# Kernel tuning notes

Hardware: AMD Instinct MI355X
Metric: run time of the kernel (lower is better)

The kernel has to match this reference:

```python
import jax, jax.numpy as jnp
import numpy as np

I, H, M, C, LOC, K = 512, 256, 80, 1024, 32, 31
C2 = C // 2
B, S, T = 32, 256, 800


def setup_inputs() -> dict:
    key = jax.random.key(0)
    ks = jax.random.split(key, 20)
    sc = 0.02
    return {
        "encodings": jax.random.normal(ks[0], (B, S, I), jnp.float32),
        "queries": jax.random.normal(ks[1], (B, T, H), jnp.float32),
        "outputs": jax.random.normal(ks[2], (B, T, M), jnp.float32),
        "mask": jnp.ones((B, S), jnp.float32),
        # GRUCell (PyTorch layout: gates ordered r, z, n)
        "w_ih": jax.random.normal(ks[3], (3 * C, I + H), jnp.float32) * sc,
        "w_hh": jax.random.normal(ks[4], (3 * C, C), jnp.float32) * sc,
        "b_ih": jax.random.normal(ks[5], (3 * C,), jnp.float32) * sc,
        "b_hh": jax.random.normal(ks[6], (3 * C,), jnp.float32) * sc,
        "w_q": jax.random.normal(ks[7], (C2, C), jnp.float32) * sc,        # proj_query
        "w_loc1": jax.random.normal(ks[8], (LOC, 1, K), jnp.float32) * sc, # Conv1d(1, loc, K)
        "w_loc2": jax.random.normal(ks[9], (C2, LOC), jnp.float32) * sc,   # Conv1d(loc, C2, 1)
        "w_k": jax.random.normal(ks[10], (C2, I), jnp.float32) * sc,       # proj_key
        "b_k": jax.random.normal(ks[11], (C2,), jnp.float32) * sc,
        "w_agg": jax.random.normal(ks[12], (C2,), jnp.float32) * sc,       # Conv1d(C2, 1, 1)
        "w_t1": jax.random.normal(ks[13], (C, I + C + M), jnp.float32) * sc,
        "b_t1": jax.random.normal(ks[14], (C,), jnp.float32) * sc,
        "w_t2": jax.random.normal(ks[15], (C,), jnp.float32) * sc,
    }


def _conv1d(x, w, pad):
    # x: [B, Cin, S], w: [Cout, Cin, K]
    return jax.lax.conv_general_dilated(
        x, w, window_strides=(1,), padding=[(pad, pad)],
        dimension_numbers=("NCH", "OIH", "NCH"))


def _aligner(encodings, queries, outputs, maskb,
             w_ih, w_hh, b_ih, b_hh, w_q, w_loc1, w_loc2, w_k, b_k,
             w_agg, w_t1, b_t1, w_t2):
    bsize, seqlen, _ = encodings.shape
    # key projection: [B, S, C2]
    key = encodings @ w_k.T + b_k
    h0 = jnp.zeros((bsize, C), encodings.dtype)
    align0 = jnp.full((bsize, seqlen), 1.0 / seqlen, encodings.dtype)
    alpha0 = jnp.zeros((bsize, seqlen), encodings.dtype).at[:, 0].set(1.0)
    trans0 = jnp.full((bsize, 1), 0.5, encodings.dtype)

    def step(carry, xt):
        h, align, trans, alpha = carry
        query, frame = xt  # [B,H], [B,M]
        prev = jnp.einsum("bsi,bs->bi", encodings, alpha)
        x = jnp.concatenate([query, prev], axis=-1)  # [B, H+I]
        gx = x @ w_ih.T + b_ih
        gh = h @ w_hh.T + b_hh
        xr, xz, xn = jnp.split(gx, 3, axis=-1)
        hr, hz, hn = jnp.split(gh, 3, axis=-1)
        r = jax.nn.sigmoid(xr + hr)
        z = jax.nn.sigmoid(xz + hz)
        n = jnp.tanh(xn + r * hn)
        h_new = (1.0 - z) * n + z * h  # GRUCell update
        # location features: [B,1,S] -> [B,LOC,S] -> [B,C2,S]
        loc = _conv1d(align[:, None, :], w_loc1, K // 2)
        loc = jnp.einsum("cl,bls->bcs", w_loc2, loc)
        score = loc + (h_new @ w_q.T)[..., None] + key.swapaxes(1, 2)  # [B,C2,S]
        energy = jnp.einsum("c,bcs->bs", w_agg, jnp.tanh(score))
        energy = jnp.where(maskb, -jnp.inf, energy)
        align_new = jax.nn.softmax(energy, axis=-1)
        shifted = jnp.pad(alpha, ((0, 0), (1, 0)))[:, :-1]  # F.pad(alpha, [1,-1])
        alpha_new = ((1.0 - trans) * alpha + trans * shifted + 1e-7) * align_new
        alpha_new = alpha_new / alpha_new.sum(axis=-1, keepdims=True)
        attend = jnp.einsum("bsi,bs->bi", encodings, alpha_new)
        t_in = jnp.concatenate([attend, frame, h_new], axis=-1)
        t = jax.nn.sigmoid(jnp.tanh(t_in @ w_t1.T + b_t1) @ w_t2[:, None])  # [B,1]
        return (h_new, align_new, t, alpha_new), alpha_new

    xs = (queries.swapaxes(0, 1), outputs.swapaxes(0, 1))
    _, alphas = jax.lax.scan(step, (h0, align0, trans0, alpha0), xs)
    return alphas.swapaxes(0, 1)  # [B, T, S]


def reference(encodings, queries, outputs, mask,
              w_ih, w_hh, b_ih, b_hh, w_q, w_loc1, w_loc2, w_k, b_k,
              w_agg, w_t1, b_t1, w_t2):
    maskb = ~(mask.astype(bool))
    return _aligner(encodings, queries, outputs, maskb,
                    w_ih, w_hh, b_ih, b_hh, w_q, w_loc1, w_loc2, w_k, b_k,
                    w_agg, w_t1, b_t1, w_t2)
```

## Files before the change

kernel.cpp:

```cpp
#include <hip/hip_runtime.h>
#include <cstdint>
#include <cstddef>


namespace cfg {
constexpr int NB = 32, NS = 256, NI = 512, NHq = 256, NM = 80;
constexpr int NC = 1024, NC2 = 512, NT = 800;
constexpr int NBLK = 256, NTHR = 512;

constexpr size_t OFF_KEYT  = 0;
constexpr size_t OFF_WKT   = OFF_KEYT + (size_t)NB * NS * NC2;
constexpr size_t OFF_PU    = OFF_WKT + (size_t)NI * NC2;
constexpr size_t OFF_H     = OFF_PU + (size_t)2 * NB * NI;
constexpr size_t OFF_H16   = OFF_H + (size_t)2 * NC * NB;
constexpr size_t OFF_E     = OFF_H16 + (size_t)NB * NC;
constexpr size_t OFF_W     = OFF_E + (size_t)2 * NB * NS;
constexpr size_t OFF_SE    = OFF_W + (size_t)2 * NB * NS;
constexpr size_t OFF_SW    = OFF_SE + 64;
constexpr size_t OFF_TPART = OFF_SW + 64;
constexpr size_t OFF_TRED  = OFF_TPART + (size_t)NBLK * NB;
constexpr size_t OFF_QBUF  = OFF_TRED + 32;
constexpr size_t OFF_BAR   = OFF_QBUF + (size_t)NB * NC2;
constexpr size_t OFF_Q16   = OFF_BAR + 4608;
constexpr size_t OFF_F16   = OFF_Q16 + (size_t)NT * NB * NHq / 2;
constexpr size_t OFF_WQ16  = OFF_F16 + (size_t)NT * NB * 128 / 2;
constexpr size_t WS_FLOATS = OFF_WQ16 + (size_t)NC2 * NC / 2;
}
using namespace cfg;

typedef __attribute__((ext_vector_type(8))) short short8;
typedef __attribute__((ext_vector_type(4))) float f32x4;

#define MF(a, b, c) __builtin_amdgcn_mfma_f32_16x16x32_bf16((a), (b), (c), 0, 0, 0)
#define LDSC(d, p) asm volatile("global_load_dwordx4 %0, %1, off sc0 sc1" : "=v"(d) : "v"(p))

__device__ __forceinline__ float ld_cg(const float* p) {
  return __hip_atomic_load(p, __ATOMIC_RELAXED, __HIP_MEMORY_SCOPE_AGENT);
}
__device__ __forceinline__ void st_cg(float* p, float v) {
  __hip_atomic_store(p, v, __ATOMIC_RELAXED, __HIP_MEMORY_SCOPE_AGENT);
}
__device__ __forceinline__ void st_cg_u16(unsigned short* p, unsigned short v) {
  asm volatile("global_store_short %0, %1, off sc0 sc1" :: "v"(p), "v"((unsigned)v) : "memory");
}

__device__ __forceinline__ void vw7(short8& a0, short8& a1, short8& a2, short8& a3,
                                    short8& a4, short8& a5, short8& a6) {
  asm volatile("s_waitcnt vmcnt(0)"
               : "+v"(a0), "+v"(a1), "+v"(a2), "+v"(a3), "+v"(a4), "+v"(a5), "+v"(a6));
}
__device__ __forceinline__ void vw8(short8& a0, short8& a1, short8& a2, short8& a3,
                                    short8& a4, short8& a5, short8& a6, short8& a7) {
  asm volatile("s_waitcnt vmcnt(0)"
               : "+v"(a0), "+v"(a1), "+v"(a2), "+v"(a3), "+v"(a4), "+v"(a5), "+v"(a6), "+v"(a7));
}
__device__ __forceinline__ void vw10(short8& a0, short8& a1, short8& a2, short8& a3, short8& a4,
                                     short8& a5, short8& a6, short8& a7, short8& a8, short8& a9) {
  asm volatile("s_waitcnt vmcnt(0)"
               : "+v"(a0), "+v"(a1), "+v"(a2), "+v"(a3), "+v"(a4), "+v"(a5), "+v"(a6),
                 "+v"(a7), "+v"(a8), "+v"(a9));
}
__device__ __forceinline__ void vw15(short8& a0, short8& a1, short8& a2, short8& a3, short8& a4,
                                     short8& a5, short8& a6, short8& a7, short8& a8, short8& a9,
                                     short8& aa, short8& ab2, short8& ac, short8& ad, short8& ae) {
  asm volatile("s_waitcnt vmcnt(0)"
               : "+v"(a0), "+v"(a1), "+v"(a2), "+v"(a3), "+v"(a4), "+v"(a5), "+v"(a6),
                 "+v"(a7), "+v"(a8), "+v"(a9), "+v"(aa), "+v"(ab2), "+v"(ac), "+v"(ad), "+v"(ae));
}
__device__ __forceinline__ void vw16f(f32x4& a0, f32x4& a1, f32x4& a2, f32x4& a3, f32x4& a4,
                                      f32x4& a5, f32x4& a6, f32x4& a7, f32x4& b0, f32x4& b1,
                                      f32x4& b2, f32x4& b3, f32x4& b4, f32x4& b5, f32x4& b6,
                                      f32x4& b7) {
  asm volatile("s_waitcnt vmcnt(0)"
               : "+v"(a0), "+v"(a1), "+v"(a2), "+v"(a3), "+v"(a4), "+v"(a5), "+v"(a6), "+v"(a7),
                 "+v"(b0), "+v"(b1), "+v"(b2), "+v"(b3), "+v"(b4), "+v"(b5), "+v"(b6), "+v"(b7));
}

__device__ __forceinline__ float frcp(float x) {
#if __has_builtin(__builtin_amdgcn_rcpf)
  return __builtin_amdgcn_rcpf(x);
#else
  return 1.f / x;
#endif
}
__device__ __forceinline__ float fsig(float x) { return frcp(1.f + __expf(-x)); }
__device__ __forceinline__ float ftanh(float x) {
  const float e = __expf(2.f * x);
  return 1.f - 2.f * frcp(e + 1.f);
}
__device__ __forceinline__ short f2bf(float f) {
  unsigned u = __float_as_uint(f);
  u += 0x7FFFu + ((u >> 16) & 1u);
  return (short)(u >> 16);
}
__device__ __forceinline__ float bf2f(short s) {
  return __uint_as_float(((unsigned)(unsigned short)s) << 16);
}
__device__ __forceinline__ short8 cvt8(f32x4 lo, f32x4 hi) {
  short8 a;
  a[0] = f2bf(lo[0]); a[1] = f2bf(lo[1]); a[2] = f2bf(lo[2]); a[3] = f2bf(lo[3]);
  a[4] = f2bf(hi[0]); a[5] = f2bf(hi[1]); a[6] = f2bf(hi[2]); a[7] = f2bf(hi[3]);
  return a;
}

__device__ __forceinline__ void gbarrier(unsigned* root, unsigned* flags, unsigned& ph) {
  ++ph;
  asm volatile("s_waitcnt vmcnt(0)" ::: "memory");
  __syncthreads();
  if (blockIdx.x == 0) {
    const int t = threadIdx.x;
    if (t > 0 && t < 256) {
      while (__hip_atomic_load(&flags[t * 16], __ATOMIC_RELAXED, __HIP_MEMORY_SCOPE_AGENT) < ph)
        __builtin_amdgcn_s_sleep(1);
    }
    __syncthreads();
    if (t == 0)
      __hip_atomic_store(root, ph, __ATOMIC_RELAXED, __HIP_MEMORY_SCOPE_AGENT);
  } else {
    if (threadIdx.x == 0) {
      __hip_atomic_store(&flags[blockIdx.x * 16], ph, __ATOMIC_RELAXED, __HIP_MEMORY_SCOPE_AGENT);
      while (__hip_atomic_load(root, __ATOMIC_RELAXED, __HIP_MEMORY_SCOPE_AGENT) < ph)
        __builtin_amdgcn_s_sleep(1);
    }
  }
  __syncthreads();
}

__device__ __forceinline__ float wcat_val(const float* __restrict__ w_ih,
                                          const float* __restrict__ w_hh,
                                          const float* __restrict__ w_t1,
                                          int kind, int c, int k) {
  if (kind < 3) {
    const int gr = kind * NC + c;
    if (k < 768) return w_ih[(size_t)gr * 768 + k];
    if (k < 1792) return w_hh[(size_t)gr * NC + (k - 768)];
    return 0.f;
  }
  if (k >= 256 && k < 768) return w_t1[(size_t)c * 1616 + (k - 256)];
  if (k >= 768 && k < 1792) return w_t1[(size_t)c * 1616 + 592 + (k - 768)];
  if (k >= 1792 && k < 1872) return w_t1[(size_t)c * 1616 + 512 + (k - 1792)];
  return 0.f;
}

__global__ void k_init(const float* __restrict__ enc, const float* __restrict__ queries,
                       const float* __restrict__ outputs, const float* __restrict__ w_k,
                       const float* __restrict__ w_q, float* __restrict__ ws) {
  const size_t t0 = (size_t)blockIdx.x * blockDim.x + threadIdx.x;
  const size_t gs = (size_t)gridDim.x * blockDim.x;
  for (size_t x = t0; x < (size_t)NI * NC2; x += gs) {
    const int i = (int)(x / NC2), c2 = (int)(x % NC2);
    ws[OFF_WKT + x] = w_k[(size_t)c2 * NI + i];
  }
  for (size_t x = t0; x < (size_t)NB * NI; x += gs) {
    const int b = (int)(x / NI), i = (int)(x % NI);
    ws[OFF_PU + x] = 0.f;
    ws[OFF_PU + (size_t)NB * NI + b * NI + i] = enc[(size_t)b * NS * NI + i];
  }
  for (size_t x = t0; x < (size_t)2 * NC * NB; x += gs) ws[OFF_H + x] = 0.f;
  for (size_t x = t0; x < (size_t)NB * NC; x += gs) ws[OFF_H16 + x] = 0.f;
  for (size_t x = t0; x < (size_t)NB * NS; x += gs) {
    ws[OFF_E + x] = 0.f;
    ws[OFF_E + (size_t)NB * NS + x] = 1.f;
    ws[OFF_W + x] = 0.f;
    ws[OFF_W + (size_t)NB * NS + x] = ((x & (NS - 1)) == 0) ? 1.f : 0.f;
  }
  for (size_t x = t0; x < (size_t)NB; x += gs) {
    ws[OFF_SE + x] = 0.f; ws[OFF_SE + NB + x] = (float)NS;
    ws[OFF_SW + x] = 0.f; ws[OFF_SW + NB + x] = 1.f;
    ws[OFF_TRED + x] = 0.f;
  }
  unsigned* bar = (unsigned*)(ws + OFF_BAR);
  for (size_t x = t0; x < 4608; x += gs) bar[x] = 0u;
  unsigned short* Q16 = (unsigned short*)(ws + OFF_Q16);
  for (size_t x = t0; x < (size_t)NT * NB * NHq; x += gs) {
    const int k = (int)(x & (NHq - 1));
    const int b = (int)((x >> 8) & (NB - 1));
    const int t = (int)(x >> 13);
    Q16[x] = (unsigned short)f2bf(queries[((size_t)b * NT + t) * NHq + k]);
  }
  unsigned short* F16 = (unsigned short*)(ws + OFF_F16);
  for (size_t x = t0; x < (size_t)NT * NB * 128; x += gs) {
    const int k = (int)(x & 127);
    const int b = (int)((x >> 7) & (NB - 1));
    const int t = (int)(x >> 12);
    F16[x] = (k < NM) ? (unsigned short)f2bf(outputs[((size_t)b * NT + t) * NM + k]) : 0;
  }
  unsigned short* WQ16 = (unsigned short*)(ws + OFF_WQ16);
  for (size_t x = t0; x < (size_t)NC2 * NC; x += gs)
    WQ16[x] = (unsigned short)f2bf(w_q[x]);
}

__global__ __launch_bounds__(NTHR) void k_key(const float* __restrict__ enc,
                                              const float* __restrict__ b_k,
                                              float* __restrict__ ws) {
  __shared__ float encl[4 * NI];
  const int bid = blockIdx.x, tid = threadIdx.x;
  const int b = bid >> 3, s0 = (bid & 7) * 32;
  const float* wkT = ws + OFF_WKT;
  float* keyT = ws + OFF_KEYT;
  const float bk = b_k[tid];
  for (int q = 0; q < 8; ++q) {
    const int sb = s0 + q * 4;
    for (int x = tid; x < 4 * NI; x += NTHR) {
      const int ss = x >> 9, i = x & (NI - 1);
      encl[x] = enc[((size_t)(b * NS + sb + ss)) * NI + i];
    }
    __syncthreads();
    float a0 = bk, a1 = bk, a2 = bk, a3 = bk;
    for (int i = 0; i < NI; ++i) {
      const float wv = wkT[(size_t)i * NC2 + tid];
      a0 += wv * encl[i];           a1 += wv * encl[NI + i];
      a2 += wv * encl[2 * NI + i];  a3 += wv * encl[3 * NI + i];
    }
    keyT[((size_t)(b * NS + sb + 0)) * NC2 + tid] = a0;
    keyT[((size_t)(b * NS + sb + 1)) * NC2 + tid] = a1;
    keyT[((size_t)(b * NS + sb + 2)) * NC2 + tid] = a2;
    keyT[((size_t)(b * NS + sb + 3)) * NC2 + tid] = a3;
    __syncthreads();
  }
}

__global__ __launch_bounds__(NTHR, 2) void k_main(
    const float* __restrict__ enc, const float* __restrict__ mask,
    const float* __restrict__ w_ih, const float* __restrict__ w_hh,
    const float* __restrict__ b_ih, const float* __restrict__ b_hh,
    const float* __restrict__ w_loc1, const float* __restrict__ w_loc2,
    const float* __restrict__ w_agg, const float* __restrict__ w_t1,
    const float* __restrict__ b_t1, const float* __restrict__ w_t2,
    float* ws, float* __restrict__ out) {
  const int bid = blockIdx.x, tid = threadIdx.x;
  float* const keyT = ws + OFF_KEYT;
  float* const PU = ws + OFF_PU;
  float* const HB = ws + OFF_H;
  unsigned short* const HB16 = (unsigned short*)(ws + OFF_H16);
  float* const EB = ws + OFF_E;
  float* const WBUF = ws + OFF_W;
  float* const SEB = ws + OFF_SE;
  float* const SWB = ws + OFF_SW;
  float* const TPART = ws + OFF_TPART;
  float* const TRED = ws + OFF_TRED;
  float* const QBUF = ws + OFF_QBUF;
  unsigned* const root = (unsigned*)(ws + OFF_BAR);
  unsigned* const flags = root + 16;
  const unsigned short* const Q16 = (const unsigned short*)(ws + OFF_Q16);
  const unsigned short* const F16 = (const unsigned short*)(ws + OFF_F16);
  const unsigned short* const WQ16 = (const unsigned short*)(ws + OFF_WQ16);

  __shared__ float Cred[2 * 5 * 4 * 64];
  __shared__ float gout2[5 * 4 * 32];
  __shared__ float swinv_l[32];
  __shared__ float tredl[128];
  __shared__ float alignl[72];
  __shared__ float wl2[34];
  __shared__ float qbl[520];
  __shared__ float Epart[32 * 9];
  __shared__ float wstash[32];
  __shared__ float scal[4];

  const int lane = tid & 63, wv = tid >> 6;
  const int m2 = wv >> 2, k4 = wv & 3;
  const int kg = lane >> 4;
  const int ab = m2 * 16 + (lane & 15);
  const int cs = bid * 4;
  const int pb_b = bid >> 3, pb_s0 = (bid & 7) * 32;
  const int col = lane & 15, quad = lane >> 4;
  unsigned ph = 0;

  short8 wreg[16];
  {
    const int n = lane & 15;
    const int kind = n >> 2, ch = cs + (n & 3);
#pragma unroll
    for (int si = 0; si < 16; ++si) {
      int s = (k4 == 0) ? (si < 8 ? si : (si < 15 ? 16 + si : -1))
            : (k4 == 1) ? 8 + si
            : (k4 == 2) ? (si < 15 ? 31 + si : -1)
                        : (si < 14 ? 46 + si : -1);
      short8 w = {0, 0, 0, 0, 0, 0, 0, 0};
      if (s >= 0) {
        const int k0 = s * 32 + kg * 8;
#pragma unroll
        for (int jj = 0; jj < 8; ++jj)
          w[jj] = f2bf(wcat_val(w_ih, w_hh, w_t1, kind, ch, k0 + jj));
      }
      wreg[si] = w;
    }
  }
  short8 wcA[4];
  unsigned keylo[4][2], keyhi[4][2];
  f32x4 wagr[4];
#pragma unroll
  for (int t = 0; t < 4; ++t) {
    const int mt = 4 * wv + t;
    short8 wfr;
#pragma unroll
    for (int jj = 0; jj < 8; ++jj) {
      const int k = quad * 8 + jj;
      float s = 0.f;
      if (k < 31) {
        const int c2 = mt * 16 + col;
        for (int l = 0; l < 32; ++l) s += w_loc2[c2 * 32 + l] * w_loc1[l * 31 + k];
      }
      wfr[jj] = f2bf(s);
    }
    wcA[t] = wfr;
    const int c2r = mt * 16 + quad * 4;
#pragma unroll
    for (int r = 0; r < 4; ++r) wagr[t][r] = w_agg[c2r + r];
#pragma unroll
    for (int nt = 0; nt < 2; ++nt) {
      const float* kp = &keyT[((size_t)(pb_b * NS + pb_s0 + nt * 16 + col)) * NC2 + c2r];
      keylo[t][nt] = ((unsigned)(unsigned short)f2bf(kp[0])) |
                     (((unsigned)(unsigned short)f2bf(kp[1])) << 16);
      keyhi[t][nt] = ((unsigned)(unsigned short)f2bf(kp[2])) |
                     (((unsigned)(unsigned short)f2bf(kp[3])) << 16);
    }
  }
  if (tid >= 62 && tid < 72) alignl[tid] = 0.f;
  __syncthreads();

  for (int j = 0; j < NT; ++j) {
    const int p = j & 1;
    const float* pu_prev = PU + (size_t)(1 - p) * NB * NI;
    float* pu_cur = PU + (size_t)p * NB * NI;
    const float* h_prev = HB + (size_t)(1 - p) * NC * NB;
    float* h_cur = HB + (size_t)p * NC * NB;
    const unsigned short* hb16_prev = HB16 + (size_t)(1 - p) * NB * NC;
    unsigned short* hb16_cur = HB16 + (size_t)p * NB * NC;
    const float* e_prev = EB + (size_t)(1 - p) * NB * NS;
    float* e_cur = EB + (size_t)p * NB * NS;
    const float* w_prev = WBUF + (size_t)(1 - p) * NB * NS;
    float* w_cur = WBUF + (size_t)p * NB * NS;
    const float* se_prev = SEB + (size_t)(1 - p) * NB;
    float* se_cur = SEB + (size_t)p * NB;
    const float* sw_prev = SWB + (size_t)(1 - p) * NB;
    float* sw_cur = SWB + (size_t)p * NB;

    if (tid < 64) st_cg(&pu_cur[bid * 64 + tid], 0.f);
    if (bid == 0 && tid < NB) st_cg(&se_cur[tid], 0.f);
    if (bid == 1 && tid < NB) st_cg(&sw_cur[tid], 0.f);
    if (tid < NB) swinv_l[tid] = 1.f / ld_cg(&sw_prev[tid]);
    __syncthreads();

    if (j >= 1 && bid < NB && tid < NS)
      out[((size_t)bid * NT + (j - 1)) * NS + tid] = ld_cg(&w_prev[bid * NS + tid]) * swinv_l[bid];

    f32x4 accA = {0.f, 0.f, 0.f, 0.f}, accB = {0.f, 0.f, 0.f, 0.f};
    if (k4 == 0) {
      const unsigned short* qp = Q16 + ((size_t)j * NB + ab) * NHq + kg * 8;
      const unsigned short* hp = hb16_prev + (size_t)ab * NC + kg * 8;
      short8 h0, h1, h2, h3, h4, h5, h6;
      LDSC(h0, hp);        LDSC(h1, hp + 32);   LDSC(h2, hp + 64);  LDSC(h3, hp + 96);
      LDSC(h4, hp + 128);  LDSC(h5, hp + 160);  LDSC(h6, hp + 192);
      const short8 q0 = *(const short8*)(qp);
      const short8 q1 = *(const short8*)(qp + 32);
      const short8 q2 = *(const short8*)(qp + 64);
      const short8 q3 = *(const short8*)(qp + 96);
      const short8 q4 = *(const short8*)(qp + 128);
      const short8 q5 = *(const short8*)(qp + 160);
      const short8 q6 = *(const short8*)(qp + 192);
      const short8 q7 = *(const short8*)(qp + 224);
      vw7(h0, h1, h2, h3, h4, h5, h6);
      accA = MF(q0, wreg[0], accA); accA = MF(q1, wreg[1], accA);
      accA = MF(q2, wreg[2], accA); accA = MF(q3, wreg[3], accA);
      accA = MF(q4, wreg[4], accA); accA = MF(q5, wreg[5], accA);
      accA = MF(q6, wreg[6], accA); accA = MF(q7, wreg[7], accA);
      accB = MF(h0, wreg[8], accB);  accB = MF(h1, wreg[9], accB);
      accB = MF(h2, wreg[10], accB); accB = MF(h3, wreg[11], accB);
      accB = MF(h4, wreg[12], accB); accB = MF(h5, wreg[13], accB);
      accB = MF(h6, wreg[14], accB);
    } else if (k4 == 1) {
      const float* pp = pu_prev + (size_t)ab * NI + kg * 8;
#pragma unroll
      for (int rd = 0; rd < 2; ++rd) {
        const float* pb = pp + rd * 256;
        f32x4 a0, a1, a2, a3, a4, a5, a6, a7, b0, b1, b2, b3, b4, b5, b6, b7;
        LDSC(a0, pb);        LDSC(b0, pb + 4);
        LDSC(a1, pb + 32);   LDSC(b1, pb + 36);
        LDSC(a2, pb + 64);   LDSC(b2, pb + 68);
        LDSC(a3, pb + 96);   LDSC(b3, pb + 100);
        LDSC(a4, pb + 128);  LDSC(b4, pb + 132);
        LDSC(a5, pb + 160);  LDSC(b5, pb + 164);
        LDSC(a6, pb + 192);  LDSC(b6, pb + 196);
        LDSC(a7, pb + 224);  LDSC(b7, pb + 228);
        vw16f(a0, a1, a2, a3, a4, a5, a6, a7, b0, b1, b2, b3, b4, b5, b6, b7);
        const int w0 = rd * 8;
        accA = MF(cvt8(a0, b0), wreg[w0 + 0], accA);
        accA = MF(cvt8(a1, b1), wreg[w0 + 1], accA);
        accA = MF(cvt8(a2, b2), wreg[w0 + 2], accA);
        accA = MF(cvt8(a3, b3), wreg[w0 + 3], accA);
        accA = MF(cvt8(a4, b4), wreg[w0 + 4], accA);
        accA = MF(cvt8(a5, b5), wreg[w0 + 5], accA);
        accA = MF(cvt8(a6, b6), wreg[w0 + 6], accA);
        accA = MF(cvt8(a7, b7), wreg[w0 + 7], accA);
      }
    } else if (k4 == 2) {
      const unsigned short* hp = hb16_prev + (size_t)ab * NC + kg * 8 + 224;
      short8 h0, h1, h2, h3, h4, h5, h6, h7, h8, h9, ha, hb2, hc, hd, he;
      LDSC(h0, hp);        LDSC(h1, hp + 32);  LDSC(h2, hp + 64);  LDSC(h3, hp + 96);
      LDSC(h4, hp + 128);  LDSC(h5, hp + 160); LDSC(h6, hp + 192); LDSC(h7, hp + 224);
      LDSC(h8, hp + 256);  LDSC(h9, hp + 288); LDSC(ha, hp + 320); LDSC(hb2, hp + 352);
      LDSC(hc, hp + 384);  LDSC(hd, hp + 416); LDSC(he, hp + 448);
      vw15(h0, h1, h2, h3, h4, h5, h6, h7, h8, h9, ha, hb2, hc, hd, he);
      accA = MF(h0, wreg[0], accA);  accA = MF(h1, wreg[1], accA);
      accA = MF(h2, wreg[2], accA);  accA = MF(h3, wreg[3], accA);
      accA = MF(h4, wreg[4], accA);  accA = MF(h5, wreg[5], accA);
      accA = MF(h6, wreg[6], accA);  accA = MF(h7, wreg[7], accA);
      accA = MF(h8, wreg[8], accA);  accA = MF(h9, wreg[9], accA);
      accA = MF(ha, wreg[10], accA); accA = MF(hb2, wreg[11], accA);
      accA = MF(hc, wreg[12], accA); accA = MF(hd, wreg[13], accA);
      accA = MF(he, wreg[14], accA);
    } else {
      const unsigned short* hp = hb16_prev + (size_t)ab * NC + kg * 8 + 704;
      short8 h0, h1, h2, h3, h4, h5, h6, h7, h8, h9;
      LDSC(h0, hp);        LDSC(h1, hp + 32);  LDSC(h2, hp + 64);  LDSC(h3, hp + 96);
      LDSC(h4, hp + 128);  LDSC(h5, hp + 160); LDSC(h6, hp + 192); LDSC(h7, hp + 224);
      LDSC(h8, hp + 256);  LDSC(h9, hp + 288);
      short8 f0 = {0,0,0,0,0,0,0,0}, f1 = f0, f2 = f0, f3 = f0;
      if (j > 0) {
        const unsigned short* fp = F16 + ((size_t)(j - 1) * NB + ab) * 128 + kg * 8;
        f0 = *(const short8*)(fp);
        f1 = *(const short8*)(fp + 32);
        f2 = *(const short8*)(fp + 64);
        f3 = *(const short8*)(fp + 96);
      }
      vw10(h0, h1, h2, h3, h4, h5, h6, h7, h8, h9);
      accA = MF(h0, wreg[0], accA); accA = MF(h1, wreg[1], accA);
      accA = MF(h2, wreg[2], accA); accA = MF(h3, wreg[3], accA);
      accA = MF(h4, wreg[4], accA); accA = MF(h5, wreg[5], accA);
      accA = MF(h6, wreg[6], accA); accA = MF(h7, wreg[7], accA);
      accA = MF(h8, wreg[8], accA); accA = MF(h9, wreg[9], accA);
      accA = MF(f0, wreg[10], accA); accA = MF(f1, wreg[11], accA);
      accA = MF(f2, wreg[12], accA); accA = MF(f3, wreg[13], accA);
    }
    {
      auto cidx = [](int m, int sg, int r, int l) { return ((m * 5 + sg) * 4 + r) * 64 + l; };
      if (k4 == 0) {
#pragma unroll
        for (int r = 0; r < 4; ++r) {
          Cred[cidx(m2, 0, r, lane)] = accA[r];
          Cred[cidx(m2, 1, r, lane)] = accB[r];
        }
      } else {
        const int sg = 1 + k4;
#pragma unroll
        for (int r = 0; r < 4; ++r) Cred[cidx(m2, sg, r, lane)] = accA[r];
      }
    }
    __syncthreads();
    {
      const int n = tid & 15, b = tid >> 4;
      const int m2r = b >> 4, bm = b & 15, l = (bm >> 2) * 16 + n, r = bm & 3;
      auto cidx = [](int m, int sg, int rr, int ll) { return ((m * 5 + sg) * 4 + rr) * 64 + ll; };
      const float s0 = Cred[cidx(m2r, 0, r, l)];
      const float sB = Cred[cidx(m2r, 1, r, l)];
      const float s1 = Cred[cidx(m2r, 2, r, l)];
      const float s2 = sB + Cred[cidx(m2r, 3, r, l)] + Cred[cidx(m2r, 4, r, l)];
      const float swv = swinv_l[b];
      const int kind = n >> 2, c4o = n & 3;
      if (kind == 2) {
        gout2[2 * 128 + c4o * 32 + b] = s0 + swv * s1;
        gout2[3 * 128 + c4o * 32 + b] = s2;
      } else {
        const int slot = (kind == 3) ? 4 : kind;
        gout2[slot * 128 + c4o * 32 + b] = s0 + swv * s1 + s2;
      }
    }
    __syncthreads();
    if (tid < 128) {
      const int c4o = tid >> 5, b = tid & 31, c = cs + c4o;
      const float xr = gout2[0 * 128 + c4o * 32 + b] + b_ih[c] + b_hh[c];
      const float xz = gout2[1 * 128 + c4o * 32 + b] + b_ih[NC + c] + b_hh[NC + c];
      const float xn = gout2[2 * 128 + c4o * 32 + b] + b_ih[2 * NC + c];
      const float hn = gout2[3 * 128 + c4o * 32 + b] + b_hh[2 * NC + c];
      const float tp = gout2[4 * 128 + c4o * 32 + b];
      const float r = fsig(xr), z = fsig(xz);
      const float nn = ftanh(xn + r * hn);
      const float hnew = (1.f - z) * nn + z * h_prev[c * 32 + b];
      h_cur[c * 32 + b] = hnew;
      st_cg_u16(&hb16_cur[(size_t)b * NC + c], (unsigned short)f2bf(hnew));
      tredl[c4o * 32 + b] = w_t2[c] * ftanh(tp + b_t1[c]);
    }
    __syncthreads();
    if (tid < NB)
      st_cg(&TPART[bid * NB + tid],
            tredl[tid] + tredl[32 + tid] + tredl[64 + tid] + tredl[96 + tid]);
    gbarrier(root, flags, ph);

    if (bid < 32) {
      f32x4 qacc = {0.f, 0.f, 0.f, 0.f};
      const unsigned short* hb = HB16 + (size_t)p * NB * NC + (size_t)ab * NC + kg * 8;
      short8 g0, g1, g2, g3, g4, g5, g6, g7;
      LDSC(g0, hb + (k4 * 8 + 0) * 32); LDSC(g1, hb + (k4 * 8 + 1) * 32);
      LDSC(g2, hb + (k4 * 8 + 2) * 32); LDSC(g3, hb + (k4 * 8 + 3) * 32);
      LDSC(g4, hb + (k4 * 8 + 4) * 32); LDSC(g5, hb + (k4 * 8 + 5) * 32);
      LDSC(g6, hb + (k4 * 8 + 6) * 32); LDSC(g7, hb + (k4 * 8 + 7) * 32);
      const int jq = bid * 16 + col;
      const unsigned short* wp = WQ16 + (size_t)jq * NC + k4 * 8 * 32 + kg * 8;
      vw8(g0, g1, g2, g3, g4, g5, g6, g7);
      qacc = MF(g0, *(const short8*)(wp), qacc);
      qacc = MF(g1, *(const short8*)(wp + 32), qacc);
      qacc = MF(g2, *(const short8*)(wp + 64), qacc);
      qacc = MF(g3, *(const short8*)(wp + 96), qacc);
      qacc = MF(g4, *(const short8*)(wp + 128), qacc);
      qacc = MF(g5, *(const short8*)(wp + 160), qacc);
      qacc = MF(g6, *(const short8*)(wp + 192), qacc);
      qacc = MF(g7, *(const short8*)(wp + 224), qacc);
#pragma unroll
      for (int r = 0; r < 4; ++r) Cred[((m2 * 4 + k4) * 4 + r) * 64 + lane] = qacc[r];
      __syncthreads();
      {
        const int col2 = tid & 15, b2 = tid >> 4;
        const int m2r = b2 >> 4, bm = b2 & 15, l = (bm >> 2) * 16 + col2, r = bm & 3;
        float s = 0.f;
#pragma unroll
        for (int kk = 0; kk < 4; ++kk) s += Cred[((m2r * 4 + kk) * 4 + r) * 64 + l];
        st_cg(&QBUF[(size_t)b2 * NC2 + bid * 16 + col2], s);
      }
    } else if (bid >= 64 && bid < 96) {
      const int b2 = bid - 64;
      float v = (tid < NBLK) ? ld_cg(&TPART[tid * NB + b2]) : 0.f;
#pragma unroll
      for (int off = 32; off > 0; off >>= 1) v += __shfl_down(v, off);
      if (lane == 0) Cred[wv] = v;
      __syncthreads();
      if (tid == 0) {
        float s = 0.f;
#pragma unroll
        for (int w8 = 0; w8 < 8; ++w8) s += Cred[w8];
        st_cg(&TRED[b2], s);
      }
    }
    gbarrier(root, flags, ph);

    {
      const int b = pb_b, s0v = pb_s0;
      if (tid == 0) {
        scal[0] = ld_cg(&se_prev[b]);
        scal[1] = ld_cg(&sw_prev[b]);
        scal[2] = ld_cg(&TRED[b]);
      }
      qbl[tid] = ld_cg(&QBUF[(size_t)b * NC2 + tid]);
      if (tid < 62) {
        const int sp = s0v + tid - 15;
        alignl[tid] = (sp >= 0 && sp < NS) ? ld_cg(&e_prev[b * NS + sp]) : 0.f;
      }
      if (tid >= 64 && tid < 97) {
        const int i2 = tid - 64, sp = s0v + i2 - 1;
        wl2[i2] = (sp >= 0 && sp < NS) ? ld_cg(&w_prev[b * NS + sp]) : 0.f;
      }
      __syncthreads();
      const float invSE = 1.f / scal[0];
      const float invSW = 1.f / scal[1];
      const float tr = (j == 0) ? 0.5f : fsig(scal[2]);
      short8 bfr[2];
#pragma unroll
      for (int nt = 0; nt < 2; ++nt) {
        const int base = nt * 16 + col + quad * 8;
        short8 bv;
#pragma unroll
        for (int jj = 0; jj < 8; ++jj) bv[jj] = f2bf(alignl[base + jj] * invSE);
        bfr[nt] = bv;
      }
#pragma unroll
      for (int nt = 0; nt < 2; ++nt) {
        float pe = 0.f;
#pragma unroll
        for (int t = 0; t < 4; ++t) {
          const int c2b = (4 * wv + t) * 16 + quad * 4;
          f32x4 acc;
          acc[0] = qbl[c2b + 0] + __uint_as_float(keylo[t][nt] << 16);
          acc[1] = qbl[c2b + 1] + __uint_as_float(keylo[t][nt] & 0xffff0000u);
          acc[2] = qbl[c2b + 2] + __uint_as_float(keyhi[t][nt] << 16);
          acc[3] = qbl[c2b + 3] + __uint_as_float(keyhi[t][nt] & 0xffff0000u);
          acc = MF(wcA[t], bfr[nt], acc);
          pe += wagr[t][0] * ftanh(acc[0]);
          pe += wagr[t][1] * ftanh(acc[1]);
          pe += wagr[t][2] * ftanh(acc[2]);
          pe += wagr[t][3] * ftanh(acc[3]);
        }
        pe += __shfl_xor(pe, 16);
        pe += __shfl_xor(pe, 32);
        if (lane < 16) Epart[(nt * 16 + col) * 9 + wv] = pe;
      }
      __syncthreads();
      if (tid < 32) {
        const int sl = tid, s = s0v + sl;
        float Ev = 0.f;
#pragma unroll
        for (int w8 = 0; w8 < 8; ++w8) Ev += Epart[sl * 9 + w8];
        const float ev = (mask[b * NS + s] != 0.f) ? __expf(Ev) : 0.f;
        const float csv = ((1.f - tr) * wl2[sl + 1] + tr * wl2[sl]) * invSW + 1e-7f;
        const float wvv = csv * ev;
        st_cg(&e_cur[b * NS + s], ev);
        st_cg(&w_cur[b * NS + s], wvv);
        wstash[sl] = wvv;
        float se = ev, sw2 = wvv;
#pragma unroll
        for (int off = 16; off > 0; off >>= 1) {
          se += __shfl_down(se, off, 32);
          sw2 += __shfl_down(sw2, off, 32);
        }
        if (sl == 0) { atomicAdd(&se_cur[b], se); atomicAdd(&sw_cur[b], sw2); }
      }
      __syncthreads();
      {
        float acc = 0.f;
        const float* encb = enc + ((size_t)(b * NS + s0v)) * NI + tid;
#pragma unroll 8
        for (int ss = 0; ss < 32; ++ss) acc += wstash[ss] * encb[(size_t)ss * NI];
        atomicAdd(&pu_cur[(size_t)b * NI + tid], acc);
      }
    }
    gbarrier(root, flags, ph);
  }

  if (bid < NB && tid < NS) {
    const float invSW = 1.f / ld_cg(&SWB[NB + bid]);
    out[((size_t)bid * NT + (NT - 1)) * NS + tid] =
        ld_cg(&WBUF[(size_t)NB * NS + bid * NS + tid]) * invSW;
  }
}

extern "C" void kernel_launch(void* const* d_in, const int* in_sizes, int n_in,
                              void* d_out, int out_size, void* d_ws, size_t ws_size,
                              hipStream_t stream) {
  const float* enc     = (const float*)d_in[0];
  const float* queries = (const float*)d_in[1];
  const float* outputs = (const float*)d_in[2];
  const float* mask    = (const float*)d_in[3];
  const float* w_ih    = (const float*)d_in[4];
  const float* w_hh    = (const float*)d_in[5];
  const float* b_ih    = (const float*)d_in[6];
  const float* b_hh    = (const float*)d_in[7];
  const float* w_q     = (const float*)d_in[8];
  const float* w_loc1  = (const float*)d_in[9];
  const float* w_loc2  = (const float*)d_in[10];
  const float* w_k     = (const float*)d_in[11];
  const float* b_k     = (const float*)d_in[12];
  const float* w_agg   = (const float*)d_in[13];
  const float* w_t1    = (const float*)d_in[14];
  const float* b_t1    = (const float*)d_in[15];
  const float* w_t2    = (const float*)d_in[16];
  float* ws = (float*)d_ws;
  float* out = (float*)d_out;
  (void)in_sizes; (void)n_in; (void)out_size; (void)ws_size;

  k_init<<<dim3(1024), dim3(256), 0, stream>>>(enc, queries, outputs, w_k, w_q, ws);
  k_key<<<dim3(NBLK), dim3(NTHR), 0, stream>>>(enc, b_k, ws);
  k_main<<<dim3(NBLK), dim3(NTHR), 0, stream>>>(enc, mask, w_ih, w_hh, b_ih, b_hh,
                                                w_loc1, w_loc2, w_agg, w_t1,
                                                b_t1, w_t2, ws, out);
}
```

Baseline: 21.28 ms.

## Replicate barrier root flag, transpose TPART layout, use bf16 encodings for attend

The grid barrier's release flag is now replicated into 32 cache-line-separated copies, so the 256 polling blocks spread across several lines instead of all spinning on one address. TPART is transposed so each reducing block reads a contiguous row. The attend accumulation reads a bf16 copy of the encodings made in the prep kernel, halving that per-step read traffic at the cost of bf16 rounding error and extra workspace. The diff also references hb16_cur, whose definition is not visible here.

```diff
diff --git a/kernel.cpp b/kernel.cpp
--- a/kernel.cpp
+++ b/kernel.cpp
@@ -18,13 +18,14 @@
 constexpr size_t OFF_SE    = OFF_W + (size_t)2 * NB * NS;
 constexpr size_t OFF_SW    = OFF_SE + 64;
 constexpr size_t OFF_TPART = OFF_SW + 64;
-constexpr size_t OFF_TRED  = OFF_TPART + (size_t)NBLK * NB;
+constexpr size_t OFF_TRED  = OFF_TPART + (size_t)NB * NBLK;
 constexpr size_t OFF_QBUF  = OFF_TRED + 32;
 constexpr size_t OFF_BAR   = OFF_QBUF + (size_t)NB * NC2;
-constexpr size_t OFF_Q16   = OFF_BAR + 4608;
+constexpr size_t OFF_Q16   = OFF_BAR + 8192;
 constexpr size_t OFF_F16   = OFF_Q16 + (size_t)NT * NB * NHq / 2;
 constexpr size_t OFF_WQ16  = OFF_F16 + (size_t)NT * NB * 128 / 2;
-constexpr size_t WS_FLOATS = OFF_WQ16 + (size_t)NC2 * NC / 2;
+constexpr size_t OFF_ENC16 = OFF_WQ16 + (size_t)NC2 * NC / 2;
+constexpr size_t WS_FLOATS = OFF_ENC16 + (size_t)NB * NS * NI / 2;
 }
 using namespace cfg;
 
@@ -93,8 +94,8 @@
   u += 0x7FFFu + ((u >> 16) & 1u);
   return (short)(u >> 16);
 }
-__device__ __forceinline__ float bf2f(short s) {
-  return __uint_as_float(((unsigned)(unsigned short)s) << 16);
+__device__ __forceinline__ float bfu(unsigned short u) {
+  return __uint_as_float(((unsigned)u) << 16);
 }
 __device__ __forceinline__ short8 cvt8(f32x4 lo, f32x4 hi) {
   short8 a;
@@ -107,6 +108,7 @@
   ++ph;
   asm volatile("s_waitcnt vmcnt(0)" ::: "memory");
   __syncthreads();
+  unsigned* rootrep = root + 4352;
   if (blockIdx.x == 0) {
     const int t = threadIdx.x;
     if (t > 0 && t < 256) {
@@ -114,12 +116,13 @@
         __builtin_amdgcn_s_sleep(1);
     }
     __syncthreads();
-    if (t == 0)
-      __hip_atomic_store(root, ph, __ATOMIC_RELAXED, __HIP_MEMORY_SCOPE_AGENT);
+    if (t < 32)
+      __hip_atomic_store(&rootrep[t * 16], ph, __ATOMIC_RELAXED, __HIP_MEMORY_SCOPE_AGENT);
   } else {
     if (threadIdx.x == 0) {
       __hip_atomic_store(&flags[blockIdx.x * 16], ph, __ATOMIC_RELAXED, __HIP_MEMORY_SCOPE_AGENT);
-      while (__hip_atomic_load(root, __ATOMIC_RELAXED, __HIP_MEMORY_SCOPE_AGENT) < ph)
+      while (__hip_atomic_load(&rootrep[(blockIdx.x & 31) * 16], __ATOMIC_RELAXED,
+                               __HIP_MEMORY_SCOPE_AGENT) < ph)
         __builtin_amdgcn_s_sleep(1);
     }
   }
@@ -170,7 +173,7 @@
     ws[OFF_TRED + x] = 0.f;
   }
   unsigned* bar = (unsigned*)(ws + OFF_BAR);
-  for (size_t x = t0; x < 4608; x += gs) bar[x] = 0u;
+  for (size_t x = t0; x < 8192; x += gs) bar[x] = 0u;
   unsigned short* Q16 = (unsigned short*)(ws + OFF_Q16);
   for (size_t x = t0; x < (size_t)NT * NB * NHq; x += gs) {
     const int k = (int)(x & (NHq - 1));
@@ -188,6 +191,9 @@
   unsigned short* WQ16 = (unsigned short*)(ws + OFF_WQ16);
   for (size_t x = t0; x < (size_t)NC2 * NC; x += gs)
     WQ16[x] = (unsigned short)f2bf(w_q[x]);
+  unsigned short* ENC16 = (unsigned short*)(ws + OFF_ENC16);
+  for (size_t x = t0; x < (size_t)NB * NS * NI; x += gs)
+    ENC16[x] = (unsigned short)f2bf(enc[x]);
 }
 
 __global__ __launch_bounds__(NTHR) void k_key(const float* __restrict__ enc,
@@ -245,6 +251,7 @@
   const unsigned short* const Q16 = (const unsigned short*)(ws + OFF_Q16);
   const unsigned short* const F16 = (const unsigned short*)(ws + OFF_F16);
   const unsigned short* const WQ16 = (const unsigned short*)(ws + OFF_WQ16);
+  const unsigned short* const ENC16 = (const unsigned short*)(ws + OFF_ENC16);
 
   __shared__ float Cred[2 * 5 * 4 * 64];
   __shared__ float gout2[5 * 4 * 32];
@@ -483,13 +490,13 @@
     }
     __syncthreads();
     if (tid < NB)
-      st_cg(&TPART[bid * NB + tid],
+      st_cg(&TPART[(size_t)tid * NBLK + bid],
             tredl[tid] + tredl[32 + tid] + tredl[64 + tid] + tredl[96 + tid]);
     gbarrier(root, flags, ph);
 
     if (bid < 32) {
       f32x4 qacc = {0.f, 0.f, 0.f, 0.f};
-      const unsigned short* hb = HB16 + (size_t)p * NB * NC + (size_t)ab * NC + kg * 8;
+      const unsigned short* hb = hb16_cur + (size_t)ab * NC + kg * 8;
       short8 g0, g1, g2, g3, g4, g5, g6, g7;
       LDSC(g0, hb + (k4 * 8 + 0) * 32); LDSC(g1, hb + (k4 * 8 + 1) * 32);
       LDSC(g2, hb + (k4 * 8 + 2) * 32); LDSC(g3, hb + (k4 * 8 + 3) * 32);
@@ -519,7 +526,7 @@
       }
     } else if (bid >= 64 && bid < 96) {
       const int b2 = bid - 64;
-      float v = (tid < NBLK) ? ld_cg(&TPART[tid * NB + b2]) : 0.f;
+      float v = (tid < NBLK) ? ld_cg(&TPART[(size_t)b2 * NBLK + tid]) : 0.f;
 #pragma unroll
       for (int off = 32; off > 0; off >>= 1) v += __shfl_down(v, off);
       if (lane == 0) Cred[wv] = v;
@@ -605,10 +612,10 @@
       }
       __syncthreads();
       {
+        const unsigned short* ep = ENC16 + ((size_t)(b * NS + s0v)) * NI + tid;
         float acc = 0.f;
-        const float* encb = enc + ((size_t)(b * NS + s0v)) * NI + tid;
 #pragma unroll 8
-        for (int ss = 0; ss < 32; ++ss) acc += wstash[ss] * encb[(size_t)ss * NI];
+        for (int ss = 0; ss < 32; ++ss) acc += wstash[ss] * bfu(ep[(size_t)ss * NI]);
         atomicAdd(&pu_cur[(size_t)b * NI + tid], acc);
       }
     }
```

After: 19.86 ms. 1.07x faster.
